# Kernel tuning notes

Measured on AMD Instinct MI355X. Metric: run time of the kernel, lower is better.

Reference implementation:

```python
import jax, jax.numpy as jnp
import numpy as np

EPS = 1e-5
CONV_THRESHOLD = 0.0


def setup_inputs() -> dict:
    key = jax.random.key(0)
    ks = jax.random.split(key, 16)
    B, F = 65536, 256
    H1, H2 = 1024, 512
    d_in = F + 1  # raw features + 1 scalar conv feature
    inp = {
        "x": jax.random.normal(ks[0], (B, F), dtype=jnp.float32),
        # layer 1: Linear(d_in, H1) + BatchNorm1d(H1)
        "W1": jax.random.normal(ks[1], (d_in, H1), dtype=jnp.float32) * (1.0 / np.sqrt(d_in)),
        "b1": jax.random.normal(ks[2], (H1,), dtype=jnp.float32) * 0.01,
        "g1": jnp.ones((H1,), jnp.float32) + 0.1 * jax.random.normal(ks[3], (H1,), dtype=jnp.float32),
        "be1": jax.random.normal(ks[4], (H1,), dtype=jnp.float32) * 0.01,
        "m1": jax.random.normal(ks[5], (H1,), dtype=jnp.float32) * 0.1,
        "v1": jax.random.uniform(ks[6], (H1,), dtype=jnp.float32, minval=0.5, maxval=1.5),
        # layer 2: Linear(H1, H2) + BatchNorm1d(H2)
        "W2": jax.random.normal(ks[7], (H1, H2), dtype=jnp.float32) * (1.0 / np.sqrt(H1)),
        "b2": jax.random.normal(ks[8], (H2,), dtype=jnp.float32) * 0.01,
        "g2": jnp.ones((H2,), jnp.float32) + 0.1 * jax.random.normal(ks[9], (H2,), dtype=jnp.float32),
        "be2": jax.random.normal(ks[10], (H2,), dtype=jnp.float32) * 0.01,
        "m2": jax.random.normal(ks[11], (H2,), dtype=jnp.float32) * 0.1,
        "v2": jax.random.uniform(ks[12], (H2,), dtype=jnp.float32, minval=0.5, maxval=1.5),
        # output head: Linear(H2, 1)
        "W3": jax.random.normal(ks[13], (H2, 1), dtype=jnp.float32) * (1.0 / np.sqrt(H2)),
        "b3": jax.random.normal(ks[14], (1,), dtype=jnp.float32) * 0.01,
    }
    return inp


def _bn(h, g, be, m, v):
    # eval-mode BatchNorm1d with running statistics
    return g * (h - m) * jax.lax.rsqrt(v + EPS) + be


def reference(x, W1, b1, g1, be1, m1, v1, W2, b2, g2, be2, m2, v2, W3, b3):
    # Batched replacement of the per-sample numpy threshold conv:
    # the Conv filter reduces the whole sample patch with a mean and thresholds it,
    # producing one binary scalar feature per sample.  [B, 1]
    conv_feat = jnp.where(jnp.mean(x, axis=1, keepdims=True) > CONV_THRESHOLD, 1.0, 0.0).astype(x.dtype)
    h = jnp.concatenate([x, conv_feat], axis=1)  # [B, F+1]
    h = jax.nn.relu(_bn(h @ W1 + b1, g1, be1, m1, v1))  # [B, H1]
    h = jax.nn.relu(_bn(h @ W2 + b2, g2, be2, m2, v2))  # [B, H2]
    return jax.nn.sigmoid(h @ W3 + b3)  # [B, 1]
```

## Files before the change

kernel.cpp:

```cpp
#include <hip/hip_runtime.h>
#include <hip/hip_bf16.h>
#include <hip/hip_cooperative_groups.h>
#include <cstdint>
#include <cstddef>

namespace cg = cooperative_groups;

typedef __bf16 bf16_t;
typedef bf16_t bf16x8 __attribute__((ext_vector_type(8)));
typedef float f32x4 __attribute__((ext_vector_type(4)));

#define BN_EPS 1e-5f

__device__ __forceinline__ void async_load16(const bf16_t* g, bf16_t* lds) {
  __builtin_amdgcn_global_load_lds(
      (__attribute__((address_space(1))) uint32_t*)(g),
      (__attribute__((address_space(3))) uint32_t*)(lds),
      16, 0, 0);
}

__global__ void prep_weights_kernel(const float* __restrict__ W1, const float* __restrict__ W2,
                                    const float* b1, const float* g1, const float* be1,
                                    const float* m1, const float* v1,
                                    const float* b2, const float* g2, const float* be2,
                                    const float* m2, const float* v2,
                                    bf16_t* __restrict__ W1T, bf16_t* __restrict__ W2T,
                                    float* s1, float* t1, float* s2, float* t2,
                                    float* w1last) {
  const int b = blockIdx.x;
  if (b < 192) {
    const float* src;
    bf16_t* dst;
    int R, C, bx, by;
    if (b < 64) { src = W1; dst = W1T; R = 256; C = 1024; bx = b & 15; by = b >> 4; }
    else        { src = W2; dst = W2T; R = 1024; C = 512; bx = (b - 64) & 7; by = (b - 64) >> 3; }
    __shared__ bf16_t tile[64][66];
    const int r0 = by * 64, c0 = bx * 64;
    const int tc = threadIdx.x & 63;
    const int tr4 = threadIdx.x >> 6;
#pragma unroll
    for (int i = 0; i < 16; ++i) {
      int r = i * 4 + tr4;
      tile[r][tc] = (bf16_t)src[(size_t)(r0 + r) * C + c0 + tc];
    }
    __syncthreads();
#pragma unroll
    for (int i = 0; i < 16; ++i) {
      int rr = i * 4 + tr4;
      dst[(size_t)(c0 + rr) * R + r0 + tc] = tile[tc][rr];
    }
  } else {
    for (int i = threadIdx.x; i < 1024; i += 256) {
      float s = g1[i] * rsqrtf(v1[i] + BN_EPS);
      s1[i] = s;
      t1[i] = be1[i] - m1[i] * s + b1[i] * s;
      w1last[i] = W1[256 * 1024 + i];
      if (i < 512) {
        float s2v = g2[i] * rsqrtf(v2[i] + BN_EPS);
        s2[i] = s2v;
        t2[i] = be2[i] - m2[i] * s2v + b2[i] * s2v;
      }
    }
  }
}

__device__ __forceinline__ void gemm1_body(
    const float* __restrict__ x, const bf16_t* __restrict__ W1T,
    const float* __restrict__ s1, const float* __restrict__ t1,
    const float* __restrict__ w1last, bf16_t* __restrict__ h1,
    unsigned char* smem, int mTile, int lane, int w) {
  bf16_t* As = (bf16_t*)smem;
  bf16_t* BsBase = (bf16_t*)(smem + 65536);
  float* convs = (float*)(smem + 65536);
  const int l15 = lane & 15;
  const int quad = lane >> 4;
  const int p = w >> 1;
  const int h = w & 1;

  {
    const int rsub = lane >> 5;
    const int c = lane & 31;
#pragma unroll
    for (int i = 0; i < 16; ++i) {
      int row = w * 32 + i * 2 + rsub;
      const float* gx = x + (size_t)(mTile + row) * 256 + c * 8;
      const float4 a = *(const float4*)gx;
      const float4 bq = *(const float4*)(gx + 4);
      float s = a.x + a.y + a.z + a.w + bq.x + bq.y + bq.z + bq.w;
      bf16x8 v = {(bf16_t)a.x, (bf16_t)a.y, (bf16_t)a.z, (bf16_t)a.w,
                  (bf16_t)bq.x, (bf16_t)bq.y, (bf16_t)bq.z, (bf16_t)bq.w};
      *(bf16x8*)(As + row * 256 + (c ^ (row & 7)) * 8) = v;
#pragma unroll
      for (int m = 1; m <= 16; m <<= 1) s += __shfl_xor(s, m);
      if (c == 0) convs[row] = (s > 0.0f) ? 1.0f : 0.0f;
    }
  }
  __syncthreads();
  float cf[4][4];
#pragma unroll
  for (int ti = 0; ti < 4; ++ti)
#pragma unroll
    for (int r = 0; r < 4; ++r)
      cf[ti][r] = convs[h * 64 + ti * 16 + quad * 4 + r];

  for (int j = 0; j < 4; ++j) {
    const int colbase = (p * 4 + j) * 128;
    f32x4 acc[4][8];
#pragma unroll
    for (int i = 0; i < 4; ++i)
#pragma unroll
      for (int t = 0; t < 8; ++t) {
        f32x4 z = {0.f, 0.f, 0.f, 0.f};
        acc[i][t] = z;
      }

    const bf16_t* gB = W1T + (size_t)(colbase + h * 64 + (lane >> 2)) * 256 + (lane & 3) * 8;
    bf16_t* lB = BsBase + p * (128 * 32) + (h * 64) * 32;

    for (int ks = 0; ks < 8; ++ks) {
      __syncthreads();
#pragma unroll
      for (int i = 0; i < 4; ++i)
        async_load16(gB + (size_t)(i * 16) * 256 + ks * 32, lB + (i * 16) * 32);
      __syncthreads();

      bf16x8 af[4], bfr[8];
#pragma unroll
      for (int ti = 0; ti < 4; ++ti) {
        int row = h * 64 + ti * 16 + l15;
        af[ti] = *(const bf16x8*)(As + row * 256 + ((ks * 4 + quad) ^ (l15 & 7)) * 8);
      }
#pragma unroll
      for (int tj = 0; tj < 8; ++tj)
        bfr[tj] = *(const bf16x8*)(BsBase + p * (128 * 32) + (tj * 16 + l15) * 32 + quad * 8);
#pragma unroll
      for (int ti = 0; ti < 4; ++ti)
#pragma unroll
        for (int tj = 0; tj < 8; ++tj)
          acc[ti][tj] = __builtin_amdgcn_mfma_f32_16x16x32_bf16(af[ti], bfr[tj], acc[ti][tj], 0, 0, 0);
    }

    float sc[8], tc[8], wl[8];
#pragma unroll
    for (int tj = 0; tj < 8; ++tj) {
      int c = colbase + tj * 16 + l15;
      sc[tj] = s1[c];
      tc[tj] = t1[c];
      wl[tj] = w1last[c];
    }
#pragma unroll
    for (int ti = 0; ti < 4; ++ti)
#pragma unroll
      for (int r = 0; r < 4; ++r) {
        int row = mTile + h * 64 + ti * 16 + quad * 4 + r;
        size_t base = (size_t)row * 1024 + colbase;
#pragma unroll
        for (int tj = 0; tj < 8; ++tj) {
          float z = acc[ti][tj][r] + cf[ti][r] * wl[tj];
          z = fmaxf(z * sc[tj] + tc[tj], 0.f);
          h1[base + tj * 16 + l15] = (bf16_t)z;
        }
      }
  }
}

__device__ __forceinline__ void gemm2_task_body(
    const bf16_t* __restrict__ h1, const bf16_t* __restrict__ W2T,
    const float* __restrict__ s2, const float* __restrict__ t2,
    const float* __restrict__ W3, float* __restrict__ partials,
    unsigned char* smem, int task, int lane, int w) {
  bf16_t* As2 = (bf16_t*)smem;
  bf16_t* Bs2 = (bf16_t*)(smem + 16384);
  const int l15 = lane & 15;
  const int quad = lane >> 4;
  const int sRow = lane >> 2;
  const int sCol = (lane & 3) * 8;

  const int mt = (task >> 5) * 8 + (task & 7);
  const int mTile2 = mt * 256;
  const int nt = (task >> 3) & 3;
  const int nTile = nt * 128;

  const bf16_t* gA = h1 + (size_t)(mTile2 + w * 64 + sRow) * 1024 + sCol;
  const bf16_t* gB = W2T + (size_t)(nTile + w * 32 + sRow) * 1024 + sCol;
  bf16_t* lA = As2 + (w * 64) * 32;
  bf16_t* lB = Bs2 + (w * 32) * 32;

  f32x4 acc[4][8];
#pragma unroll
  for (int i = 0; i < 4; ++i)
#pragma unroll
    for (int j = 0; j < 8; ++j) {
      f32x4 z = {0.f, 0.f, 0.f, 0.f};
      acc[i][j] = z;
    }

  for (int k0 = 0; k0 < 1024; k0 += 32) {
    async_load16(gA + k0, lA);
    async_load16(gA + (size_t)16 * 1024 + k0, lA + 16 * 32);
    async_load16(gA + (size_t)32 * 1024 + k0, lA + 32 * 32);
    async_load16(gA + (size_t)48 * 1024 + k0, lA + 48 * 32);
    async_load16(gB + k0, lB);
    async_load16(gB + (size_t)16 * 1024 + k0, lB + 16 * 32);
    __syncthreads();

    bf16x8 af[4], bfr[8];
#pragma unroll
    for (int t = 0; t < 4; ++t)
      af[t] = *(const bf16x8*)(As2 + (w * 64 + t * 16 + l15) * 32 + quad * 8);
#pragma unroll
    for (int t = 0; t < 8; ++t)
      bfr[t] = *(const bf16x8*)(Bs2 + (t * 16 + l15) * 32 + quad * 8);
#pragma unroll
    for (int ti = 0; ti < 4; ++ti)
#pragma unroll
      for (int tj = 0; tj < 8; ++tj)
        acc[ti][tj] = __builtin_amdgcn_mfma_f32_16x16x32_bf16(af[ti], bfr[tj], acc[ti][tj], 0, 0, 0);
    __syncthreads();
  }

  float sc[8], tc[8], w3c[8];
#pragma unroll
  for (int tj = 0; tj < 8; ++tj) {
    int c = nTile + tj * 16 + l15;
    sc[tj] = s2[c];
    tc[tj] = t2[c];
    w3c[tj] = W3[c];
  }
#pragma unroll
  for (int ti = 0; ti < 4; ++ti)
#pragma unroll
    for (int r = 0; r < 4; ++r) {
      float pv = 0.f;
#pragma unroll
      for (int tj = 0; tj < 8; ++tj) {
        float z = fmaxf(acc[ti][tj][r] * sc[tj] + tc[tj], 0.f);
        pv += z * w3c[tj];
      }
#pragma unroll
      for (int m = 1; m <= 8; m <<= 1) pv += __shfl_xor(pv, m);
      if (l15 == 0)
        partials[(size_t)nt * 65536 + mTile2 + w * 64 + ti * 16 + quad * 4 + r] = pv;
    }
}

__global__ __launch_bounds__(256, 2) void gemm1_kernel(
    const float* __restrict__ x, const bf16_t* __restrict__ W1T,
    const float* __restrict__ s1, const float* __restrict__ t1,
    const float* __restrict__ w1last, bf16_t* __restrict__ h1) {
  __shared__ __align__(16) unsigned char smem[81920];
  gemm1_body(x, W1T, s1, t1, w1last, h1, smem, blockIdx.x * 128,
             threadIdx.x & 63, threadIdx.x >> 6);
}

__global__ __launch_bounds__(256, 2) void gemm2_kernel(
    const bf16_t* __restrict__ h1, const bf16_t* __restrict__ W2T,
    const float* __restrict__ s2, const float* __restrict__ t2,
    const float* __restrict__ W3, float* __restrict__ partials) {
  __shared__ __align__(16) unsigned char smem[24576];
  gemm2_task_body(h1, W2T, s2, t2, W3, partials, smem, blockIdx.x,
                  threadIdx.x & 63, threadIdx.x >> 6);
}

__global__ void sigmoid_partials_kernel(const float* __restrict__ partials,
                                        const float* __restrict__ b3,
                                        float* __restrict__ out) {
  int i = blockIdx.x * 256 + threadIdx.x;
  float z = partials[i] + partials[65536 + i] + partials[2 * 65536 + i] +
            partials[3 * 65536 + i] + b3[0];
  out[i] = 1.0f / (1.0f + expf(-z));
}

__global__ __launch_bounds__(256, 2) void fused_mlp_coop(
    const float* __restrict__ x,
    const bf16_t* __restrict__ W1T, const bf16_t* __restrict__ W2T,
    const float* __restrict__ s1, const float* __restrict__ t1,
    const float* __restrict__ w1last,
    const float* __restrict__ s2, const float* __restrict__ t2,
    const float* __restrict__ W3, const float* __restrict__ b3,
    bf16_t* __restrict__ h1, float* __restrict__ partials,
    float* __restrict__ out) {
  __shared__ __align__(16) unsigned char smem[81920];
  cg::grid_group grid = cg::this_grid();
  const int tid = threadIdx.x;
  const int lane = tid & 63;
  const int w = tid >> 6;

  gemm1_body(x, W1T, s1, t1, w1last, h1, smem, blockIdx.x * 128, lane, w);

  grid.sync();

  gemm2_task_body(h1, W2T, s2, t2, W3, partials, smem, blockIdx.x, lane, w);
  gemm2_task_body(h1, W2T, s2, t2, W3, partials, smem, blockIdx.x + 512, lane, w);

  grid.sync();

  if (tid < 128) {
    int r = blockIdx.x * 128 + tid;
    float z = partials[r] + partials[65536 + r] + partials[2 * 65536 + r] +
              partials[3 * 65536 + r] + b3[0];
    out[r] = 1.0f / (1.0f + expf(-z));
  }
}

extern "C" void kernel_launch(void* const* d_in, const int* in_sizes, int n_in,
                              void* d_out, int out_size, void* d_ws, size_t ws_size,
                              hipStream_t stream) {
  const float* x = (const float*)d_in[0];
  const float* W1 = (const float*)d_in[1];
  const float* b1 = (const float*)d_in[2];
  const float* g1 = (const float*)d_in[3];
  const float* be1 = (const float*)d_in[4];
  const float* m1 = (const float*)d_in[5];
  const float* v1 = (const float*)d_in[6];
  const float* W2 = (const float*)d_in[7];
  const float* b2 = (const float*)d_in[8];
  const float* g2 = (const float*)d_in[9];
  const float* be2 = (const float*)d_in[10];
  const float* m2 = (const float*)d_in[11];
  const float* v2 = (const float*)d_in[12];
  const float* W3 = (const float*)d_in[13];
  const float* b3 = (const float*)d_in[14];
  float* out = (float*)d_out;

  char* p = (char*)d_ws;
  bf16_t* h1 = (bf16_t*)p;       p += (size_t)65536 * 1024 * 2;
  float* partials = (float*)p;   p += (size_t)4 * 65536 * 4;
  bf16_t* W1T = (bf16_t*)p;      p += (size_t)1024 * 256 * 2;
  bf16_t* W2T = (bf16_t*)p;      p += (size_t)512 * 1024 * 2;
  float* w1last = (float*)p;     p += 1024 * 4;
  float* s1 = (float*)p;         p += 1024 * 4;
  float* t1 = (float*)p;         p += 1024 * 4;
  float* s2 = (float*)p;         p += 512 * 4;
  float* t2 = (float*)p;         p += 512 * 4;

  prep_weights_kernel<<<193, 256, 0, stream>>>(W1, W2, b1, g1, be1, m1, v1,
                                               b2, g2, be2, m2, v2,
                                               W1T, W2T, s1, t1, s2, t2, w1last);

  int dev = 0;
  (void)hipGetDevice(&dev);
  int coopOk = 0;
  (void)hipDeviceGetAttribute(&coopOk, hipDeviceAttributeCooperativeLaunch, dev);
  int numCU = 0;
  (void)hipDeviceGetAttribute(&numCU, hipDeviceAttributeMultiprocessorCount, dev);
  int maxBlk = 0;
  (void)hipOccupancyMaxActiveBlocksPerMultiprocessor(&maxBlk, fused_mlp_coop, 256, 0);

  bool useCoop = (coopOk != 0) && ((long)maxBlk * (long)numCU >= 512L);
  if (useCoop) {
    void* args[] = {(void*)&x, (void*)&W1T, (void*)&W2T, (void*)&s1, (void*)&t1,
                    (void*)&w1last, (void*)&s2, (void*)&t2, (void*)&W3, (void*)&b3,
                    (void*)&h1, (void*)&partials, (void*)&out};
    hipError_t e = hipLaunchCooperativeKernel((const void*)fused_mlp_coop,
                                              dim3(512), dim3(256), args, 0, stream);
    if (e != hipSuccess) useCoop = false;
  }
  if (!useCoop) {
    gemm1_kernel<<<512, 256, 0, stream>>>(x, W1T, s1, t1, w1last, h1);
    gemm2_kernel<<<1024, 256, 0, stream>>>(h1, W2T, s2, t2, W3, partials);
    sigmoid_partials_kernel<<<256, 256, 0, stream>>>(partials, b3, out);
  }
}
```

Before: 251.2 us.

## Load W1 fragments directly from global and double-buffer GEMM2 LDS staging

In the first GEMM, the W1 tile is no longer staged through LDS with two barriers per k-step. Each wave now reads its B fragments straight from global memory, which removes the barriers and shrinks the LDS footprint. In the second GEMM, the single-buffered LDS staging becomes a double buffer: the next k-slice is prefetched asynchronously while MFMAs run on the current one, with one barrier per step. The risks are more global/L2 traffic and uncoalesced 16-byte reads for W1 (each wave pair now reads the same W1 tile), plus larger LDS use for GEMM2.

```diff
diff --git a/kernel.cpp b/kernel.cpp
--- a/kernel.cpp
+++ b/kernel.cpp
@@ -70,7 +70,6 @@
     const float* __restrict__ w1last, bf16_t* __restrict__ h1,
     unsigned char* smem, int mTile, int lane, int w) {
   bf16_t* As = (bf16_t*)smem;
-  bf16_t* BsBase = (bf16_t*)(smem + 65536);
   float* convs = (float*)(smem + 65536);
   const int l15 = lane & 15;
   const int quad = lane >> 4;
@@ -114,25 +113,20 @@
         acc[i][t] = z;
       }
 
-    const bf16_t* gB = W1T + (size_t)(colbase + h * 64 + (lane >> 2)) * 256 + (lane & 3) * 8;
-    bf16_t* lB = BsBase + p * (128 * 32) + (h * 64) * 32;
-
+    const bf16_t* gB = W1T + (size_t)(colbase + l15) * 256 + quad * 8;
+
+#pragma unroll
     for (int ks = 0; ks < 8; ++ks) {
-      __syncthreads();
-#pragma unroll
-      for (int i = 0; i < 4; ++i)
-        async_load16(gB + (size_t)(i * 16) * 256 + ks * 32, lB + (i * 16) * 32);
-      __syncthreads();
-
-      bf16x8 af[4], bfr[8];
+      bf16x8 bfr[8];
+#pragma unroll
+      for (int tj = 0; tj < 8; ++tj)
+        bfr[tj] = *(const bf16x8*)(gB + (size_t)(tj * 16) * 256 + ks * 32);
+      bf16x8 af[4];
 #pragma unroll
       for (int ti = 0; ti < 4; ++ti) {
         int row = h * 64 + ti * 16 + l15;
         af[ti] = *(const bf16x8*)(As + row * 256 + ((ks * 4 + quad) ^ (l15 & 7)) * 8);
       }
-#pragma unroll
-      for (int tj = 0; tj < 8; ++tj)
-        bfr[tj] = *(const bf16x8*)(BsBase + p * (128 * 32) + (tj * 16 + l15) * 32 + quad * 8);
 #pragma unroll
       for (int ti = 0; ti < 4; ++ti)
 #pragma unroll
@@ -170,7 +164,7 @@
     const float* __restrict__ W3, float* __restrict__ partials,
     unsigned char* smem, int task, int lane, int w) {
   bf16_t* As2 = (bf16_t*)smem;
-  bf16_t* Bs2 = (bf16_t*)(smem + 16384);
+  bf16_t* Bs2 = (bf16_t*)(smem + 32768);
   const int l15 = lane & 15;
   const int quad = lane >> 4;
   const int sRow = lane >> 2;
@@ -183,8 +177,8 @@
 
   const bf16_t* gA = h1 + (size_t)(mTile2 + w * 64 + sRow) * 1024 + sCol;
   const bf16_t* gB = W2T + (size_t)(nTile + w * 32 + sRow) * 1024 + sCol;
-  bf16_t* lA = As2 + (w * 64) * 32;
-  bf16_t* lB = Bs2 + (w * 32) * 32;
+  bf16_t* lA0 = As2 + (w * 64) * 32;
+  bf16_t* lB0 = Bs2 + (w * 32) * 32;
 
   f32x4 acc[4][8];
 #pragma unroll
@@ -195,29 +189,46 @@
       acc[i][j] = z;
     }
 
+  __syncthreads();
+
+#define STAGE2(buf, k0)                                                     \
+  do {                                                                      \
+    bf16_t* lA = lA0 + (buf)*8192;                                          \
+    bf16_t* lB = lB0 + (buf)*4096;                                          \
+    async_load16(gA + (k0), lA);                                            \
+    async_load16(gA + (size_t)16 * 1024 + (k0), lA + 16 * 32);              \
+    async_load16(gA + (size_t)32 * 1024 + (k0), lA + 32 * 32);              \
+    async_load16(gA + (size_t)48 * 1024 + (k0), lA + 48 * 32);              \
+    async_load16(gB + (k0), lB);                                            \
+    async_load16(gB + (size_t)16 * 1024 + (k0), lB + 16 * 32);              \
+  } while (0)
+
+  STAGE2(0, 0);
+  __syncthreads();
+
+  int buf = 0;
   for (int k0 = 0; k0 < 1024; k0 += 32) {
-    async_load16(gA + k0, lA);
-    async_load16(gA + (size_t)16 * 1024 + k0, lA + 16 * 32);
-    async_load16(gA + (size_t)32 * 1024 + k0, lA + 32 * 32);
-    async_load16(gA + (size_t)48 * 1024 + k0, lA + 48 * 32);
-    async_load16(gB + k0, lB);
-    async_load16(gB + (size_t)16 * 1024 + k0, lB + 16 * 32);
-    __syncthreads();
+    if (k0 + 32 < 1024) STAGE2(buf ^ 1, k0 + 32);
 
     bf16x8 af[4], bfr[8];
 #pragma unroll
     for (int t = 0; t < 4; ++t)
-      af[t] = *(const bf16x8*)(As2 + (w * 64 + t * 16 + l15) * 32 + quad * 8);
+      af[t] = *(const bf16x8*)(As2 + buf * 8192 + (w * 64 + t * 16 + l15) * 32 + quad * 8);
 #pragma unroll
     for (int t = 0; t < 8; ++t)
-      bfr[t] = *(const bf16x8*)(Bs2 + (t * 16 + l15) * 32 + quad * 8);
+      bfr[t] = *(const bf16x8*)(Bs2 + buf * 4096 + (t * 16 + l15) * 32 + quad * 8);
 #pragma unroll
     for (int ti = 0; ti < 4; ++ti)
 #pragma unroll
       for (int tj = 0; tj < 8; ++tj)
         acc[ti][tj] = __builtin_amdgcn_mfma_f32_16x16x32_bf16(af[ti], bfr[tj], acc[ti][tj], 0, 0, 0);
-    __syncthreads();
-  }
+
+    if (k0 + 32 < 1024) {
+      __syncthreads();
+      buf ^= 1;
+    }
+  }
+#undef STAGE2
 
   float sc[8], tc[8], w3c[8];
 #pragma unroll
@@ -248,7 +259,7 @@
     const float* __restrict__ x, const bf16_t* __restrict__ W1T,
     const float* __restrict__ s1, const float* __restrict__ t1,
     const float* __restrict__ w1last, bf16_t* __restrict__ h1) {
-  __shared__ __align__(16) unsigned char smem[81920];
+  __shared__ __align__(16) unsigned char smem[66048];
   gemm1_body(x, W1T, s1, t1, w1last, h1, smem, blockIdx.x * 128,
              threadIdx.x & 63, threadIdx.x >> 6);
 }
@@ -257,7 +268,7 @@
     const bf16_t* __restrict__ h1, const bf16_t* __restrict__ W2T,
     const float* __restrict__ s2, const float* __restrict__ t2,
     const float* __restrict__ W3, float* __restrict__ partials) {
-  __shared__ __align__(16) unsigned char smem[24576];
+  __shared__ __align__(16) unsigned char smem[49152];
   gemm2_task_body(h1, W2T, s2, t2, W3, partials, smem, blockIdx.x,
                   threadIdx.x & 63, threadIdx.x >> 6);
 }
@@ -280,7 +291,7 @@
     const float* __restrict__ W3, const float* __restrict__ b3,
     bf16_t* __restrict__ h1, float* __restrict__ partials,
     float* __restrict__ out) {
-  __shared__ __align__(16) unsigned char smem[81920];
+  __shared__ __align__(16) unsigned char smem[66048];
   cg::grid_group grid = cg::this_grid();
   const int tid = threadIdx.x;
   const int lane = tid & 63;
```

After: 312.1 us. 24.2% more time.
